# Performance work log

Hardware: AMD Instinct MI355X
Metric: run time of the kernel (lower is better)

Reference implementation:

```python
import jax, jax.numpy as jnp
import numpy as np

DIM = 64
NUM_EXPERTS = 4
TOP_K = 2


def _dwconv3x3(x, w, b):
    # x: [B, C, H, W], w: [C, 1, 3, 3] depthwise (groups=C), b: [C]
    y = jax.lax.conv_general_dilated(
        x, w, window_strides=(1, 1), padding='SAME',
        feature_group_count=x.shape[1],
        dimension_numbers=('NCHW', 'OIHW', 'NCHW'))
    return y + b[None, :, None, None]


def setup_inputs() -> dict:
    key = jax.random.key(0)
    ks = jax.random.split(key, 12)
    B, H, W = 8, 128, 128
    s = 0.02
    return {
        'x': jax.random.normal(ks[0], (B, 2 * DIM, H, W), jnp.float32),
        'pre_w': jax.random.normal(ks[1], (DIM, 2 * DIM), jnp.float32) * s,
        'pre_b': jax.random.normal(ks[2], (DIM,), jnp.float32) * s,
        'gate_w0': jax.random.normal(ks[3], (NUM_EXPERTS, DIM), jnp.float32) * s,
        'gate_b0': jax.random.normal(ks[4], (NUM_EXPERTS,), jnp.float32) * s,
        'gate_w1': jax.random.normal(ks[5], (NUM_EXPERTS, DIM), jnp.float32) * s,
        'gate_b1': jax.random.normal(ks[6], (NUM_EXPERTS,), jnp.float32) * s,
        'exp_w1': jax.random.normal(ks[7], (NUM_EXPERTS, DIM, 1, 3, 3), jnp.float32) * s,
        'exp_b1': jax.random.normal(ks[8], (NUM_EXPERTS, DIM), jnp.float32) * s,
        'exp_w2': jax.random.normal(ks[9], (NUM_EXPERTS, DIM, 1, 3, 3), jnp.float32) * s,
        'exp_b2': jax.random.normal(ks[10], (NUM_EXPERTS, DIM), jnp.float32) * s,
    }


def reference(x, pre_w, pre_b, gate_w0, gate_b0, gate_w1, gate_b1,
              exp_w1, exp_b1, exp_w2, exp_b2):
    # pre_fuse: 1x1 conv [2*dim -> dim]
    x = jnp.einsum('bchw,oc->bohw', x, pre_w) + pre_b[None, :, None, None]

    # --- GateNetwork ---
    pooled = jnp.max(x, axis=(2, 3)) + jnp.mean(x, axis=(2, 3))  # [B, dim]
    logits = jax.nn.leaky_relu(pooled @ gate_w1.T + gate_b1, 0.2)  # [B, E]
    noise = jax.nn.softplus(pooled @ gate_w0.T + gate_b0)          # [B, E]
    n_mean = jnp.mean(noise, axis=1, keepdims=True)
    n_std = jnp.std(noise, axis=1, keepdims=True, ddof=1)          # unbiased like torch.std
    scores = logits + (noise - n_mean) / n_std
    _, topk_idx = jax.lax.top_k(scores, TOP_K)                     # [B, k]
    B = logits.shape[0]
    mask = jnp.zeros_like(logits).at[jnp.arange(B)[:, None], topk_idx].set(1.0)
    masked = jnp.where(mask > 0, logits, -jnp.inf)
    cof = jax.nn.softmax(masked, axis=1)                           # [B, E]

    # --- experts: dwconv3x3 -> GELU -> dwconv3x3, combined by gating coeffs ---
    def expert_fn(w1, b1, w2, b2):
        h = _dwconv3x3(x, w1, b1)
        h = jax.nn.gelu(h, approximate=False)
        return _dwconv3x3(h, w2, b2)

    outs = jax.vmap(expert_fn)(exp_w1, exp_b1, exp_w2, exp_b2)     # [E, B, dim, H, W]
    out = jnp.einsum('ebchw,be->bchw', outs, cof)
    return out
```

## Files before the change

kernel.cpp:

```cpp
#include <hip/hip_runtime.h>
#include <hip/hip_bf16.h>
#include <math.h>

#define HW 16384
#define IMG 128
#define C_IN 128
#define C_OUT 64
#define NB 8
#define NE 4

typedef __attribute__((ext_vector_type(8))) short bf16x8;
typedef __attribute__((ext_vector_type(4))) float f32x4;

static __device__ __forceinline__ float bf2f_u(unsigned hbits) {
  union { unsigned u; float f; } v; v.u = hbits << 16;
  return v.f;
}
static __device__ __forceinline__ float bf2f_hi(unsigned w) {
  union { unsigned u; float f; } v; v.u = w & 0xFFFF0000u;
  return v.f;
}
static __device__ __forceinline__ unsigned cvtpk(float a, float b) {
  __hip_bfloat162 p = __float22bfloat162_rn(make_float2(a, b));
  union { __hip_bfloat162 h; unsigned u; } v; v.h = p;
  return v.u;
}
static __device__ __forceinline__ void pk2(float a, float b,
                                           unsigned& hi, unsigned& lo) {
  hi = cvtpk(a, b);
  float ra = a - bf2f_u(hi & 0xFFFFu);
  float rb = b - bf2f_u(hi >> 16);
  lo = cvtpk(ra, rb);
}

union FragU { unsigned u[4]; uint4 q; bf16x8 v; };

#define ASYNC_LOAD16(gsrc, ldst)                                              \
  __builtin_amdgcn_global_load_lds(                                           \
      (const __attribute__((address_space(1))) void*)(gsrc),                  \
      (__attribute__((address_space(3))) void*)(ldst), 16, 0, 0)

__global__ __launch_bounds__(64, 4) void prefuse_mfma(
    const float* __restrict__ x, const float* __restrict__ pre_w,
    const float* __restrict__ pre_b, unsigned short* __restrict__ x1,
    float* __restrict__ pmax, float* __restrict__ psum) {
  __shared__ float xls[4][1056];
  __shared__ unsigned short tbuf[16][72];
  int lane = threadIdx.x;
  int rowb = lane & 15;
  int kg = lane >> 4;
  int blk = blockIdx.x;
  int b = blk >> 9;
  int strip = blk & 511;
  int px0 = strip << 5;

  const float* xbase = x + (size_t)b * C_IN * HW + px0;

#define STAGE(ks, bf)                                                         \
  {                                                                           \
    _Pragma("unroll")                                                         \
    for (int r = 0; r < 4; ++r) {                                             \
      int ch = (ks) * 32 + r * 8 + (lane >> 3);                               \
      ASYNC_LOAD16(xbase + (size_t)ch * HW + (lane & 7) * 4,                  \
                   &xls[bf][r * 264]);                                        \
    }                                                                         \
  }

  STAGE(0, 0)
  STAGE(1, 1)
  STAGE(2, 2)

  f32x4 acc[2][4];
#pragma unroll
  for (int ot = 0; ot < 4; ++ot) {
    float t = pre_b[ot * 16 + rowb];
#pragma unroll
    for (int pt = 0; pt < 2; ++pt) acc[pt][ot] = (f32x4){t, t, t, t};
  }

#pragma unroll
  for (int k = 0; k < 4; ++k) {
    FragU wh[4], wl[4];
#pragma unroll
    for (int ot = 0; ot < 4; ++ot) {
      const float* wp = pre_w + (ot * 16 + rowb) * C_IN + k * 32 + kg * 8;
      float4 a = *(const float4*)wp;
      float4 cq = *(const float4*)(wp + 4);
      pk2(a.x, a.y, wh[ot].u[0], wl[ot].u[0]);
      pk2(a.z, a.w, wh[ot].u[1], wl[ot].u[1]);
      pk2(cq.x, cq.y, wh[ot].u[2], wl[ot].u[2]);
      pk2(cq.z, cq.w, wh[ot].u[3], wl[ot].u[3]);
    }
    if (k == 0) {
      STAGE(3, 3)
      asm volatile("s_waitcnt vmcnt(12)" ::: "memory");
    } else if (k == 1) {
      asm volatile("s_waitcnt vmcnt(8)" ::: "memory");
    } else if (k == 2) {
      asm volatile("s_waitcnt vmcnt(4)" ::: "memory");
    } else {
      asm volatile("s_waitcnt vmcnt(0)" ::: "memory");
    }
    const float* xb = xls[k];
#pragma unroll
    for (int pt = 0; pt < 2; ++pt) {
      float xv[8];
#pragma unroll
      for (int j = 0; j < 8; ++j)
        xv[j] = xb[kg * 264 + j * 32 + pt * 16 + rowb];
      FragU h, l;
      pk2(xv[0], xv[1], h.u[0], l.u[0]);
      pk2(xv[2], xv[3], h.u[1], l.u[1]);
      pk2(xv[4], xv[5], h.u[2], l.u[2]);
      pk2(xv[6], xv[7], h.u[3], l.u[3]);
#pragma unroll
      for (int ot = 0; ot < 4; ++ot) {
        acc[pt][ot] = __builtin_amdgcn_mfma_f32_16x16x32_bf16(h.v, wh[ot].v, acc[pt][ot], 0, 0, 0);
        acc[pt][ot] = __builtin_amdgcn_mfma_f32_16x16x32_bf16(l.v, wh[ot].v, acc[pt][ot], 0, 0, 0);
        acc[pt][ot] = __builtin_amdgcn_mfma_f32_16x16x32_bf16(h.v, wl[ot].v, acc[pt][ot], 0, 0, 0);
      }
    }
  }
#undef STAGE

#pragma unroll
  for (int ot = 0; ot < 4; ++ot) {
    float m = -INFINITY, s = 0.f;
#pragma unroll
    for (int pt = 0; pt < 2; ++pt)
#pragma unroll
      for (int r = 0; r < 4; ++r) {
        float v = acc[pt][ot][r];
        m = fmaxf(m, v); s += v;
      }
    m = fmaxf(m, __shfl_xor(m, 16)); s += __shfl_xor(s, 16);
    m = fmaxf(m, __shfl_xor(m, 32)); s += __shfl_xor(s, 32);
    if (lane < 16) {
      int idx = strip * 512 + b * 64 + ot * 16 + lane;
      pmax[idx] = m; psum[idx] = s;
    }
#pragma unroll
    for (int pt = 0; pt < 2; ++pt) {
      uint2 p;
      p.x = cvtpk(acc[pt][ot][0], acc[pt][ot][1]);
      p.y = cvtpk(acc[pt][ot][2], acc[pt][ot][3]);
      *(uint2*)&tbuf[rowb][pt * 16 + kg * 4] = p;
    }
    __syncthreads();
    uint4 val = *(const uint4*)&tbuf[lane >> 2][(lane & 3) * 8];
    unsigned short* op = x1 + ((size_t)b * C_OUT + ot * 16 + (lane >> 2)) * HW
                            + px0 + (lane & 3) * 8;
    *(uint4*)op = val;
    __syncthreads();
  }
}

__global__ __launch_bounds__(1024) void pool_gate_kernel(
    const float* __restrict__ pmax, const float* __restrict__ psum,
    const float* __restrict__ gw0, const float* __restrict__ gb0,
    const float* __restrict__ gw1, const float* __restrict__ gb1,
    float* __restrict__ cof) {
  __shared__ float rm[16][64], rs[16][64], pooled[64];
  int b = blockIdx.x;
  int t = threadIdx.x;
  int o = t & 63, g = t >> 6;
  float m = -INFINITY, s = 0.f;
#pragma unroll
  for (int i = 0; i < 32; ++i) {
    int idx = (g * 32 + i) * 512 + b * 64 + o;
    m = fmaxf(m, pmax[idx]);
    s += psum[idx];
  }
  rm[g][o] = m; rs[g][o] = s;
  __syncthreads();
  if (t < 64) {
    float mm = rm[0][t], ss = rs[0][t];
#pragma unroll
    for (int g2 = 1; g2 < 16; ++g2) {
      mm = fmaxf(mm, rm[g2][t]);
      ss += rs[g2][t];
    }
    pooled[t] = mm + ss * (1.0f / HW);

    int lane = t;
    float pv = pooled[lane];
    float acc[8];
#pragma unroll
    for (int e = 0; e < NE; ++e) {
      acc[e]     = pv * gw0[e * C_OUT + lane];
      acc[4 + e] = pv * gw1[e * C_OUT + lane];
    }
#pragma unroll
    for (int d = 32; d >= 1; d >>= 1)
#pragma unroll
      for (int q = 0; q < 8; ++q) acc[q] += __shfl_xor(acc[q], d);

    if (lane == 0) {
      float logits[NE], noise[NE];
#pragma unroll
      for (int e = 0; e < NE; ++e) {
        float d0 = acc[e] + gb0[e];
        float d1 = acc[4 + e] + gb1[e];
        logits[e] = d1 > 0.f ? d1 : 0.2f * d1;
        noise[e] = log1pf(expf(d0));
      }
      float mn = 0.25f * (noise[0] + noise[1] + noise[2] + noise[3]);
      float var = 0.f;
#pragma unroll
      for (int e = 0; e < NE; ++e) { float d = noise[e] - mn; var += d * d; }
      float sd = sqrtf(var * (1.0f / 3.0f));
      float scores[NE];
#pragma unroll
      for (int e = 0; e < NE; ++e) scores[e] = logits[e] + (noise[e] - mn) / sd;
      int i0 = 0;
#pragma unroll
      for (int e = 1; e < NE; ++e) if (scores[e] > scores[i0]) i0 = e;
      int i1 = -1;
#pragma unroll
      for (int e = 0; e < NE; ++e)
        if (e != i0 && (i1 < 0 || scores[e] > scores[i1])) i1 = e;
      float mm2 = fmaxf(logits[i0], logits[i1]);
      float e0 = expf(logits[i0] - mm2), e1 = expf(logits[i1] - mm2);
      float inv = 1.0f / (e0 + e1);
#pragma unroll
      for (int e = 0; e < NE; ++e) cof[b * NE + e] = 0.f;
      cof[b * NE + i0] = e0 * inv;
      cof[b * NE + i1] = e1 * inv;
    }
  }
}

__global__ __launch_bounds__(256) void expert_kernel(
    const unsigned short* __restrict__ x1, const float* __restrict__ ew1,
    const float* __restrict__ eb1, const float* __restrict__ ew2,
    const float* __restrict__ eb2, const float* __restrict__ cof,
    float* __restrict__ out) {
  __shared__ unsigned short xs[132][136];
  int tid = threadIdx.x, blk = blockIdx.x;
  int c = blk & 63, b = blk >> 6;
  const unsigned short* xp = x1 + ((size_t)b * C_OUT + c) * HW;

  int eA = -1, eB = -1; float cfA = 0.f, cfB = 0.f;
#pragma unroll
  for (int e = 0; e < NE; ++e) {
    float cv = cof[b * NE + e];
    if (cv != 0.f) { if (eA < 0) { eA = e; cfA = cv; } else { eB = e; cfB = cv; } }
  }
  if (eA < 0) { eA = 0; cfA = 0.f; }
  if (eB < 0) { eB = eA; cfB = 0.f; }

  float w1A[9], w1B[9], w2A[9], w2B[9];
#pragma unroll
  for (int t = 0; t < 9; ++t) {
    w1A[t] = ew1[((size_t)eA * C_OUT + c) * 9 + t];
    w1B[t] = ew1[((size_t)eB * C_OUT + c) * 9 + t];
    w2A[t] = cfA * ew2[((size_t)eA * C_OUT + c) * 9 + t];
    w2B[t] = cfB * ew2[((size_t)eB * C_OUT + c) * 9 + t];
  }
  float b1A = eb1[eA * C_OUT + c], b1B = eb1[eB * C_OUT + c];
  float bias2 = cfA * eb2[eA * C_OUT + c] + cfB * eb2[eB * C_OUT + c];

  for (int i = tid; i < 128 * 17; i += 256) {
    int r = i / 17, j = i - r * 17;
    uint4 cur = make_uint4(0u, 0u, 0u, 0u);
    if (j < 16) cur = *(const uint4*)(xp + r * IMG + j * 8);
    unsigned prevw = (j > 0) ? ((const uint4*)(xp + r * IMG + (j - 1) * 8))->w : 0u;
    uint4 o; o.x = prevw; o.y = cur.x; o.z = cur.y; o.w = cur.z;
    *(uint4*)&xs[r + 2][j * 8] = o;
  }
  for (int i = tid; i < 4 * 17; i += 256) {
    int rr = i / 17, j = i - rr * 17;
    int r = (rr < 2) ? rr : 128 + rr;
    *(uint4*)&xs[r][j * 8] = make_uint4(0u, 0u, 0u, 0u);
  }
  __syncthreads();

  int pr = tid >> 5, pc = tid & 31;
  int px0 = pc * 4;

  float X[3][8];
#define LOADROW(slot, rowidx)                                                 \
  {                                                                           \
    const unsigned short* xr = &xs[rowidx][px0];                              \
    uint2 a = *(const uint2*)xr;                                              \
    uint2 bq = *(const uint2*)(xr + 4);                                       \
    X[slot][0] = bf2f_u(a.x & 0xFFFFu);  X[slot][1] = bf2f_hi(a.x);           \
    X[slot][2] = bf2f_u(a.y & 0xFFFFu);  X[slot][3] = bf2f_hi(a.y);           \
    X[slot][4] = bf2f_u(bq.x & 0xFFFFu); X[slot][5] = bf2f_hi(bq.x);          \
    X[slot][6] = bf2f_u(bq.y & 0xFFFFu); X[slot][7] = bf2f_hi(bq.y);          \
  }

#pragma unroll 1
  for (int rt = 0; rt < 4; ++rt) {
    int ty0 = rt * 32;
    int xrb = ty0 + pr * 4;

    float acc[4][4];
#pragma unroll
    for (int r = 0; r < 4; ++r)
#pragma unroll
      for (int cc = 0; cc < 4; ++cc) acc[r][cc] = bias2;

    LOADROW(0, xrb)
    LOADROW(1, xrb + 1)

#pragma unroll
    for (int k = 0; k < 6; ++k) {
      LOADROW((k + 2) % 3, xrb + k + 2)
      bool rowok = (unsigned)(ty0 + pr * 4 - 1 + k) < 128u;
      float hA[6], hB[6];
#pragma unroll
      for (int j = 0; j < 6; ++j) {
        float sA = b1A, sB = b1B;
#pragma unroll
        for (int dy = 0; dy < 3; ++dy) {
          const float* xw = X[(k + dy) % 3];
#pragma unroll
          for (int dx = 0; dx < 3; ++dx) {
            float xv = xw[j + dx];
            sA = fmaf(xv, w1A[dy * 3 + dx], sA);
            sB = fmaf(xv, w1B[dy * 3 + dx], sB);
          }
        }
        float uA = sA * sA, uB = sB * sB;
        float tA = fmaf(uA, fmaf(uA, 0.025f, -0.16666667f), 1.0f);
        float tB = fmaf(uB, fmaf(uB, 0.025f, -0.16666667f), 1.0f);
        float gA = sA * fmaf(0.3989422804f * sA, tA, 0.5f);
        float gB = sB * fmaf(0.3989422804f * sB, tB, 0.5f);
        bool ok = rowok && ((unsigned)(px0 - 1 + j) < 128u);
        hA[j] = ok ? gA : 0.f;
        hB[j] = ok ? gB : 0.f;
      }
#pragma unroll
      for (int dy = 0; dy < 3; ++dy) {
        int r = k - dy;
        if (r >= 0 && r < 4) {
#pragma unroll
          for (int cc = 0; cc < 4; ++cc) {
            float a = acc[r][cc];
            a = fmaf(hA[cc],     w2A[dy * 3 + 0], a);
            a = fmaf(hA[cc + 1], w2A[dy * 3 + 1], a);
            a = fmaf(hA[cc + 2], w2A[dy * 3 + 2], a);
            a = fmaf(hB[cc],     w2B[dy * 3 + 0], a);
            a = fmaf(hB[cc + 1], w2B[dy * 3 + 1], a);
            a = fmaf(hB[cc + 2], w2B[dy * 3 + 2], a);
            acc[r][cc] = a;
          }
        }
      }
    }

    float* op = out + ((size_t)b * C_OUT + c) * HW + (ty0 + pr * 4) * IMG + px0;
#pragma unroll
    for (int r = 0; r < 4; ++r)
      *(float4*)(op + r * IMG) = make_float4(acc[r][0], acc[r][1], acc[r][2], acc[r][3]);
  }
#undef LOADROW
}

extern "C" void kernel_launch(void* const* d_in, const int* in_sizes, int n_in,
                              void* d_out, int out_size, void* d_ws, size_t ws_size,
                              hipStream_t stream) {
  const float* x     = (const float*)d_in[0];
  const float* pre_w = (const float*)d_in[1];
  const float* pre_b = (const float*)d_in[2];
  const float* gw0   = (const float*)d_in[3];
  const float* gb0   = (const float*)d_in[4];
  const float* gw1   = (const float*)d_in[5];
  const float* gb1   = (const float*)d_in[6];
  const float* ew1   = (const float*)d_in[7];
  const float* eb1   = (const float*)d_in[8];
  const float* ew2   = (const float*)d_in[9];
  const float* eb2   = (const float*)d_in[10];
  float* out = (float*)d_out;

  char* ws = (char*)d_ws;
  unsigned short* x1 = (unsigned short*)ws;
  float* pmax = (float*)(ws + 16777216);
  float* psum = (float*)(ws + 17825792);
  float* cof  = (float*)(ws + 18874368);

  prefuse_mfma<<<4096, 64, 0, stream>>>(x, pre_w, pre_b, x1, pmax, psum);
  pool_gate_kernel<<<8, 1024, 0, stream>>>(pmax, psum, gw0, gb0, gw1, gb1, cof);
  expert_kernel<<<512, 256, 0, stream>>>(x1, ew1, eb1, ew2, eb2, cof, out);
}
```

Before: 71.47 us.

## Widen pre-fuse blocks to eight waves with shared double-buffered LDS staging

The 1x1 pre-fuse MFMA kernel now runs 512-thread blocks of eight waves covering 256 pixels, instead of 4096 single-wave blocks covering 32 pixels. Input channels are staged cooperatively into a padded, double-buffered LDS tile, and the explicit four-deep vmcnt prefetch is replaced by block barriers. The intent is more coalesced wide loads and fewer, larger blocks. The cost is shallower prefetch depth, barrier stalls, and about 64KB of LDS per block, which limits occupancy. The per-wave output transpose buffer reuses the staging memory.

```diff
diff --git a/kernel.cpp b/kernel.cpp
--- a/kernel.cpp
+++ b/kernel.cpp
@@ -40,35 +40,34 @@
       (const __attribute__((address_space(1))) void*)(gsrc),                  \
       (__attribute__((address_space(3))) void*)(ldst), 16, 0, 0)
 
-__global__ __launch_bounds__(64, 4) void prefuse_mfma(
+__global__ __launch_bounds__(512) void prefuse_mfma(
     const float* __restrict__ x, const float* __restrict__ pre_w,
     const float* __restrict__ pre_b, unsigned short* __restrict__ x1,
     float* __restrict__ pmax, float* __restrict__ psum) {
-  __shared__ float xls[4][1056];
-  __shared__ unsigned short tbuf[16][72];
-  int lane = threadIdx.x;
+  __shared__ float xbuf[2][32 * 257];
+  int tid = threadIdx.x;
+  int w = tid >> 6, lane = tid & 63;
   int rowb = lane & 15;
   int kg = lane >> 4;
   int blk = blockIdx.x;
-  int b = blk >> 9;
-  int strip = blk & 511;
-  int px0 = strip << 5;
+  int b = blk >> 6;
+  int strip = blk & 63;
+  int px0 = strip << 8;
+  int pxw = w << 5;
 
   const float* xbase = x + (size_t)b * C_IN * HW + px0;
 
 #define STAGE(ks, bf)                                                         \
   {                                                                           \
     _Pragma("unroll")                                                         \
-    for (int r = 0; r < 4; ++r) {                                             \
-      int ch = (ks) * 32 + r * 8 + (lane >> 3);                               \
-      ASYNC_LOAD16(xbase + (size_t)ch * HW + (lane & 7) * 4,                  \
-                   &xls[bf][r * 264]);                                        \
+    for (int i = 0; i < 4; ++i) {                                             \
+      int cl = (w << 2) + i;                                                  \
+      ASYNC_LOAD16(xbase + (size_t)((ks) * 32 + cl) * HW + lane * 4,          \
+                   &xbuf[bf][cl * 257]);                                      \
     }                                                                         \
   }
 
   STAGE(0, 0)
-  STAGE(1, 1)
-  STAGE(2, 2)
 
   f32x4 acc[2][4];
 #pragma unroll
@@ -78,8 +77,12 @@
     for (int pt = 0; pt < 2; ++pt) acc[pt][ot] = (f32x4){t, t, t, t};
   }
 
+  __syncthreads();
+
 #pragma unroll
   for (int k = 0; k < 4; ++k) {
+    if (k < 3) STAGE(k + 1, (k + 1) & 1)
+
     FragU wh[4], wl[4];
 #pragma unroll
     for (int ot = 0; ot < 4; ++ot) {
@@ -91,23 +94,14 @@
       pk2(cq.x, cq.y, wh[ot].u[2], wl[ot].u[2]);
       pk2(cq.z, cq.w, wh[ot].u[3], wl[ot].u[3]);
     }
-    if (k == 0) {
-      STAGE(3, 3)
-      asm volatile("s_waitcnt vmcnt(12)" ::: "memory");
-    } else if (k == 1) {
-      asm volatile("s_waitcnt vmcnt(8)" ::: "memory");
-    } else if (k == 2) {
-      asm volatile("s_waitcnt vmcnt(4)" ::: "memory");
-    } else {
-      asm volatile("s_waitcnt vmcnt(0)" ::: "memory");
-    }
-    const float* xb = xls[k];
+
+    const float* xb = xbuf[k & 1];
 #pragma unroll
     for (int pt = 0; pt < 2; ++pt) {
       float xv[8];
 #pragma unroll
       for (int j = 0; j < 8; ++j)
-        xv[j] = xb[kg * 264 + j * 32 + pt * 16 + rowb];
+        xv[j] = xb[(kg * 8 + j) * 257 + pxw + pt * 16 + rowb];
       FragU h, l;
       pk2(xv[0], xv[1], h.u[0], l.u[0]);
       pk2(xv[2], xv[3], h.u[1], l.u[1]);
@@ -120,9 +114,11 @@
         acc[pt][ot] = __builtin_amdgcn_mfma_f32_16x16x32_bf16(h.v, wl[ot].v, acc[pt][ot], 0, 0, 0);
       }
     }
+    __syncthreads();
   }
 #undef STAGE
 
+  unsigned short* tbuf = (unsigned short*)(&xbuf[0][0]) + w * 1280;
 #pragma unroll
   for (int ot = 0; ot < 4; ++ot) {
     float m = -INFINITY, s = 0.f;
@@ -136,7 +132,7 @@
     m = fmaxf(m, __shfl_xor(m, 16)); s += __shfl_xor(s, 16);
     m = fmaxf(m, __shfl_xor(m, 32)); s += __shfl_xor(s, 32);
     if (lane < 16) {
-      int idx = strip * 512 + b * 64 + ot * 16 + lane;
+      int idx = (strip * 8 + w) * 512 + b * 64 + ot * 16 + lane;
       pmax[idx] = m; psum[idx] = s;
     }
 #pragma unroll
@@ -144,12 +140,12 @@
       uint2 p;
       p.x = cvtpk(acc[pt][ot][0], acc[pt][ot][1]);
       p.y = cvtpk(acc[pt][ot][2], acc[pt][ot][3]);
-      *(uint2*)&tbuf[rowb][pt * 16 + kg * 4] = p;
+      *(uint2*)&tbuf[rowb * 72 + pt * 16 + kg * 4] = p;
     }
     __syncthreads();
-    uint4 val = *(const uint4*)&tbuf[lane >> 2][(lane & 3) * 8];
+    uint4 val = *(const uint4*)&tbuf[(lane >> 2) * 72 + (lane & 3) * 8];
     unsigned short* op = x1 + ((size_t)b * C_OUT + ot * 16 + (lane >> 2)) * HW
-                            + px0 + (lane & 3) * 8;
+                            + px0 + pxw + (lane & 3) * 8;
     *(uint4*)op = val;
     __syncthreads();
   }
@@ -380,7 +376,7 @@
   float* psum = (float*)(ws + 17825792);
   float* cof  = (float*)(ws + 18874368);
 
-  prefuse_mfma<<<4096, 64, 0, stream>>>(x, pre_w, pre_b, x1, pmax, psum);
+  prefuse_mfma<<<512, 512, 0, stream>>>(x, pre_w, pre_b, x1, pmax, psum);
   pool_gate_kernel<<<8, 1024, 0, stream>>>(pmax, psum, gw0, gb0, gw1, gb1, cof);
   expert_kernel<<<512, 256, 0, stream>>>(x1, ew1, eb1, ew2, eb2, cof, out);
 }
```

Result: slower. 75.42 us (+5.5%).
